# Kernel optimization log

Hardware: AMD Instinct MI355X
Metric: run time of the kernel (lower is better)

The kernel has to match this reference:

```python
import jax, jax.numpy as jnp
import numpy as np

B, L, H = 8, 2048, 1024
MASK_IDENTITY = True


def setup_inputs() -> dict:
    key = jax.random.key(0)
    ks = jax.random.split(key, 7)
    s = 1.0 / np.sqrt(H)
    return {
        "x": jax.random.normal(ks[0], (B, L, H), dtype=jnp.float32),
        "Wq": jax.random.uniform(ks[1], (H, H), jnp.float32, -s, s),
        "bq": jax.random.uniform(ks[2], (H,), jnp.float32, -s, s),
        "Wk": jax.random.uniform(ks[3], (H, H), jnp.float32, -s, s),
        "bk": jax.random.uniform(ks[4], (H,), jnp.float32, -s, s),
        "Wv": jax.random.uniform(ks[5], (H, H), jnp.float32, -s, s),
        "bv": jax.random.uniform(ks[6], (H,), jnp.float32, -s, s),
    }


def reference(x, Wq, bq, Wk, bk, Wv, bv):
    # Linear layers (torch Linear: y = x @ W.T + b)
    q = jnp.einsum("blh,oh->blo", x, Wq) + bq
    k = jnp.einsum("blh,oh->blo", x, Wk) + bk
    v = jnp.einsum("blh,oh->blo", x, Wv) + bv
    hidden = q.shape[-1]
    # NOTE: original scales by hidden_size, not sqrt(hidden_size)
    attn = jnp.einsum("blh,bmh->blm", q / hidden, k)  # [B, L, L]
    if MASK_IDENTITY:
        mask_value = -jnp.finfo(attn.dtype).max
        eye = jnp.eye(attn.shape[-1], dtype=bool)  # [L, L]
        attn = jnp.where(eye[None, :, :], mask_value, attn)
    attn = jax.nn.softmax(attn, axis=-1)
    return jnp.einsum("blm,bmh->blh", attn, v)
```

## Files before the change

kernel.cpp:

```cpp
#include <hip/hip_runtime.h>


typedef unsigned short u16;
typedef __bf16 bfx8 __attribute__((ext_vector_type(8)));
typedef float f32x4 __attribute__((ext_vector_type(4)));

__device__ __forceinline__ u16 f2bf(float f) {
    unsigned int x = __float_as_uint(f);
    unsigned int r = (x + 0x7fffu + ((x >> 16) & 1u)) >> 16;
    return (u16)r;
}
__device__ __forceinline__ float bf2f(u16 u) {
    return __uint_as_float(((unsigned int)u) << 16);
}

__global__ void f32_to_bf16(const float* __restrict__ src, u16* __restrict__ dst, int n8) {
    int i = blockIdx.x * blockDim.x + threadIdx.x;
    if (i < n8) {
        float4 a = ((const float4*)src)[i * 2];
        float4 b = ((const float4*)src)[i * 2 + 1];
        ushort4 lo; lo.x = f2bf(a.x); lo.y = f2bf(a.y); lo.z = f2bf(a.z); lo.w = f2bf(a.w);
        ushort4 hi; hi.x = f2bf(b.x); hi.y = f2bf(b.y); hi.z = f2bf(b.z); hi.w = f2bf(b.w);
        ((ushort4*)dst)[i * 2] = lo;
        ((ushort4*)dst)[i * 2 + 1] = hi;
    }
}

__global__ void transpose_bf16(const u16* __restrict__ src, u16* __restrict__ dst) {
    __shared__ u16 s[64][64 + 8];
    int z = blockIdx.z;
    int tm = blockIdx.x * 64;
    int th = blockIdx.y * 64;
    const u16* sp = src + (long)z * 2048 * 1024;
    u16* dp = dst + (long)z * 1024 * 2048;
    int t = threadIdx.x;
#pragma unroll
    for (int p = 0; p < 4; ++p) {
        int r = p * 16 + (t >> 4);
        int c = (t & 15) * 4;
        ushort4 v = *(const ushort4*)(sp + (long)(tm + r) * 1024 + th + c);
        s[r][c] = v.x; s[r][c + 1] = v.y; s[r][c + 2] = v.z; s[r][c + 3] = v.w;
    }
    __syncthreads();
#pragma unroll
    for (int p = 0; p < 4; ++p) {
        int hr = p * 16 + (t >> 4);
        int c = (t & 15) * 4;
        ushort4 v;
        v.x = s[c][hr]; v.y = s[c + 1][hr]; v.z = s[c + 2][hr]; v.w = s[c + 3][hr];
        *(ushort4*)(dp + (long)(th + hr) * 2048 + tm + c) = v;
    }
}


#define FENCE asm volatile("" ::: "memory")
#define BAR   __builtin_amdgcn_s_barrier()
#define PRIO1 __builtin_amdgcn_s_setprio(1)
#define PRIO0 __builtin_amdgcn_s_setprio(0)
#define VMC(N) asm volatile("s_waitcnt vmcnt(" #N ")" ::: "memory")

#define STAGE_HALF(DST, SRC, LD, tt, h) do{ \
    _Pragma("unroll") \
    for (int rnd = 0; rnd < 2; ++rnd) { \
        int c_ = rnd * 512 + tid; \
        int row_ = (h) * 128 + (c_ >> 3); \
        int slot_ = c_ & 7; \
        const u16* g_ = (SRC) + (long)row_ * (LD) + (tt) * 64 + ((slot_ ^ (row_ & 7)) << 3); \
        char* l_ = (char*)(DST) + (h) * 16384 + rnd * 8192 + wid * 1024; \
        __builtin_amdgcn_global_load_lds((__attribute__((address_space(1))) void*)g_, \
            (__attribute__((address_space(3))) void*)l_, 16, 0, 0); \
    } \
}while(0)

#define RD_A4(dst, SARR, mibase) do{ \
    const char* _b = (const char*)(SARR) + ((wr * 128 + (mibase) * 16 + rA) * 128); \
    dst[0][0] = *(const bfx8*)(_b + 0 * 2048 + ofk0); dst[0][1] = *(const bfx8*)(_b + 0 * 2048 + ofk1); \
    dst[1][0] = *(const bfx8*)(_b + 1 * 2048 + ofk0); dst[1][1] = *(const bfx8*)(_b + 1 * 2048 + ofk1); \
    dst[2][0] = *(const bfx8*)(_b + 2 * 2048 + ofk0); dst[2][1] = *(const bfx8*)(_b + 2 * 2048 + ofk1); \
    dst[3][0] = *(const bfx8*)(_b + 3 * 2048 + ofk0); dst[3][1] = *(const bfx8*)(_b + 3 * 2048 + ofk1); \
}while(0)

#define RD_B2(dst, SARR, nibase) do{ \
    const char* _b = (const char*)(SARR) + ((wc * 64 + (nibase) * 16 + rA) * 128); \
    dst[0][0] = *(const bfx8*)(_b + 0 * 2048 + ofk0); dst[0][1] = *(const bfx8*)(_b + 0 * 2048 + ofk1); \
    dst[1][0] = *(const bfx8*)(_b + 1 * 2048 + ofk0); dst[1][1] = *(const bfx8*)(_b + 1 * 2048 + ofk1); \
}while(0)

#define MMQ(AS, BS, M0, N0) do{ \
    _Pragma("unroll") \
    for (int ks = 0; ks < 2; ++ks) \
    _Pragma("unroll") \
    for (int mi = 0; mi < 4; ++mi) \
    _Pragma("unroll") \
    for (int ni = 0; ni < 2; ++ni) \
        acc[(M0)+mi][(N0)+ni] = __builtin_amdgcn_mfma_f32_16x16x32_bf16(AS[mi][ks], BS[ni][ks], acc[(M0)+mi][(N0)+ni], 0, 0, 0); \
}while(0)

#define TILE(SA_c, SB_c, SA_o, SB_o, tt) do{ \
     \
    RD_B2(b01, SB_c, 0); RD_B2(b23, SB_c, 2); \
    if ((tt) + 1 < NT) STAGE_HALF(SB_o, B, ldb, (tt) + 1, 0); \
    FENCE; BAR; PRIO1; MMQ(aA, b01, 0, 0); PRIO0; FENCE; BAR; \
     \
    RD_A4(aB, SA_c, 4); \
    if ((tt) + 1 < NT) STAGE_HALF(SB_o, B, ldb, (tt) + 1, 1); \
    FENCE; BAR; PRIO1; MMQ(aA, b23, 0, 2); PRIO0; FENCE; BAR; \
     \
    if ((tt) + 2 < NT) STAGE_HALF(SA_c, A, lda, (tt) + 2, 0); \
    VMC(6); \
    FENCE; BAR; PRIO1; MMQ(aB, b23, 4, 2); PRIO0; FENCE; BAR; \
     \
    RD_A4(aA, SA_o, 0); \
    if ((tt) + 2 < NT) STAGE_HALF(SA_c, A, lda, (tt) + 2, 1); \
    VMC(4); \
    FENCE; BAR; PRIO1; MMQ(aB, b01, 4, 0); PRIO0; FENCE; BAR; \
}while(0)

template <int MODE>
__global__ __launch_bounds__(512, 2) void gemm8p(
    const u16* __restrict__ Ab, const u16* __restrict__ Bb,
    int K, int lda, int ldb,
    long strideA, long strideB,
    const float* __restrict__ biasCat,
    u16* __restrict__ outBf, long strideP,
    float* __restrict__ den,
    float* __restrict__ outF)
{
    __shared__ __align__(16) u16 sA0[16384];
    __shared__ __align__(16) u16 sB0[16384];
    __shared__ __align__(16) u16 sA1[16384];
    __shared__ __align__(16) u16 sB1[16384];

    const int tid  = threadIdx.x;
    const int lane = tid & 63;
    const int wid  = tid >> 6;
    const int wr = wid >> 2, wc = wid & 3;
    const int z = blockIdx.z;
    const u16* A = Ab + (long)z * strideA + (long)blockIdx.x * 256 * lda;
    const u16* B = Bb + (long)z * strideB + (long)blockIdx.y * 256 * ldb;
    const int NT = K >> 6;

    const int rA  = lane & 15;
    const int cg  = lane >> 4;
    const int swz = rA & 7;
    const int ofk0 = ((cg)     ^ swz) << 4;
    const int ofk1 = ((cg | 4) ^ swz) << 4;

    f32x4 acc[8][4] = {};
    bfx8 aA[4][2], aB[4][2], b01[2][2], b23[2][2];

    STAGE_HALF(sA0, A, lda, 0, 0); STAGE_HALF(sA0, A, lda, 0, 1);
    STAGE_HALF(sB0, B, ldb, 0, 0); STAGE_HALF(sB0, B, ldb, 0, 1);
    STAGE_HALF(sA1, A, lda, 1, 0); STAGE_HALF(sA1, A, lda, 1, 1);
    VMC(4);
    BAR;
    RD_A4(aA, sA0, 0);
    FENCE;

    for (int t = 0; t < NT; t += 2) {
        TILE(sA0, sB0, sA1, sB1, t);
        TILE(sA1, sB1, sA0, sB0, t + 1);
    }

    const int r0 = blockIdx.x * 256 + wr * 128 + (cg << 2);
    const int c0 = blockIdx.y * 256 + wc * 64 + rA;
#pragma unroll
    for (int mi = 0; mi < 8; ++mi) {
#pragma unroll
        for (int r = 0; r < 4; ++r) {
            const int grow = r0 + mi * 16 + r;
            if constexpr (MODE == 0) {
#pragma unroll
                for (int ni = 0; ni < 4; ++ni) {
                    int gcol = c0 + ni * 16;
                    float v = acc[mi][ni][r] + biasCat[gcol];
                    if (gcol < 1024) v *= (1.0f / 1024.0f);
                    int which = gcol >> 10;
                    long dst = (long)which * (16384L * 1024) + (long)grow * 1024 + (gcol & 1023);
                    outBf[dst] = f2bf(v);
                }
            } else if constexpr (MODE == 1) {
                float s = 0.0f;
#pragma unroll
                for (int ni = 0; ni < 4; ++ni) {
                    int gcol = c0 + ni * 16;
                    float p = (grow == gcol) ? 0.0f : __expf(acc[mi][ni][r]);
                    u16 pb = f2bf(p);
                    outBf[(long)z * strideP + (long)grow * 2048 + gcol] = pb;
                    s += bf2f(pb);
                }
                s += __shfl_xor(s, 1); s += __shfl_xor(s, 2);
                s += __shfl_xor(s, 4); s += __shfl_xor(s, 8);
                if (rA == 0) atomicAdd(&den[z * 2048 + grow], s);
            } else {
                float d = den[z * 2048 + grow];
#pragma unroll
                for (int ni = 0; ni < 4; ++ni)
                    outF[(long)z * (2048L * 1024) + (long)grow * 1024 + (c0 + ni * 16)] = acc[mi][ni][r] / d;
            }
        }
    }
}

extern "C" void kernel_launch(void* const* d_in, const int* in_sizes, int n_in,
                              void* d_out, int out_size, void* d_ws, size_t ws_size,
                              hipStream_t stream) {
    const float* x  = (const float*)d_in[0];
    const float* Wq = (const float*)d_in[1];
    const float* bq = (const float*)d_in[2];
    const float* Wk = (const float*)d_in[3];
    const float* bk = (const float*)d_in[4];
    const float* Wv = (const float*)d_in[5];
    const float* bv = (const float*)d_in[6];
    float* out = (float*)d_out;

    const long XB_OFF   = 0;
    const long WB_OFF   = 33554432;
    const long BIAS_OFF = WB_OFF + 6291456;
    const long DEN_OFF  = BIAS_OFF + 12288;
    const long QKV_OFF  = DEN_OFF + 65536;
    const long PB_OFF   = QKV_OFF + 2L * 33554432;
    const unsigned long long NEED = (unsigned long long)(PB_OFF + 67108864);
    if (ws_size < NEED) return;

    char* ws = (char*)d_ws;
    u16*   xb      = (u16*)(ws + XB_OFF);
    u16*   vT      = (u16*)(ws + XB_OFF);
    u16*   Wb      = (u16*)(ws + WB_OFF);
    float* biasCat = (float*)(ws + BIAS_OFF);
    float* den     = (float*)(ws + DEN_OFF);
    u16*   qkv     = (u16*)(ws + QKV_OFF);
    u16*   qb = qkv;
    u16*   kb = qkv + 16384L * 1024;
    u16*   vb = qkv + 2L * 16384 * 1024;
    u16*   Pb = (u16*)(ws + PB_OFF);

    f32_to_bf16<<<8192, 256, 0, stream>>>(x, xb, 2097152);
    f32_to_bf16<<<512, 256, 0, stream>>>(Wq, Wb, 131072);
    f32_to_bf16<<<512, 256, 0, stream>>>(Wk, Wb + 1048576, 131072);
    f32_to_bf16<<<512, 256, 0, stream>>>(Wv, Wb + 2097152, 131072);
    hipMemcpyAsync(biasCat,        bq, 4096, hipMemcpyDeviceToDevice, stream);
    hipMemcpyAsync(biasCat + 1024, bk, 4096, hipMemcpyDeviceToDevice, stream);
    hipMemcpyAsync(biasCat + 2048, bv, 4096, hipMemcpyDeviceToDevice, stream);
    hipMemsetAsync(den, 0, 65536, stream);

    gemm8p<0><<<dim3(64, 12, 1), 512, 0, stream>>>(
        xb, Wb, 1024, 1024, 1024, 0, 0, biasCat, qkv, 0, nullptr, nullptr);

    transpose_bf16<<<dim3(32, 16, 8), 256, 0, stream>>>(vb, vT);

    gemm8p<1><<<dim3(8, 8, 8), 512, 0, stream>>>(
        qb, kb, 1024, 1024, 1024, 2048L * 1024, 2048L * 1024,
        nullptr, Pb, 2048L * 2048, den, nullptr);

    gemm8p<2><<<dim3(8, 4, 8), 512, 0, stream>>>(
        Pb, vT, 2048, 2048, 2048, 2048L * 2048, 1024L * 2048,
        nullptr, nullptr, 0, den, out);
}
```

Baseline: 413.8 us.

## Compute V transposed directly via swapped GEMM, reorder tile pipeline, remap workgroups

Drops the separate V transpose kernel and instead computes V^T with a new GEMM mode that swaps operands (Wv times x), writing a bf16 transposed output with per-row bias. The main GEMM loop is also reordered: B fragments are prefetched one step earlier and the vmcnt waits are moved. The LDS swizzle gains an extra XOR bit to cut bank conflicts, and workgroup IDs are remapped in groups of eight for better L2/XCD locality. The workspace layout changes so Pb reuses the xb region. This risks correctness in the new swizzle and wait counts, and the QK projection grid shrinks from 12 to 8 column tiles.

After: 519.5 us. 25.6% more time.

```diff
diff --git a/kernel.cpp b/kernel.cpp
--- a/kernel.cpp
+++ b/kernel.cpp
@@ -26,33 +26,6 @@
     }
 }
 
-__global__ void transpose_bf16(const u16* __restrict__ src, u16* __restrict__ dst) {
-    __shared__ u16 s[64][64 + 8];
-    int z = blockIdx.z;
-    int tm = blockIdx.x * 64;
-    int th = blockIdx.y * 64;
-    const u16* sp = src + (long)z * 2048 * 1024;
-    u16* dp = dst + (long)z * 1024 * 2048;
-    int t = threadIdx.x;
-#pragma unroll
-    for (int p = 0; p < 4; ++p) {
-        int r = p * 16 + (t >> 4);
-        int c = (t & 15) * 4;
-        ushort4 v = *(const ushort4*)(sp + (long)(tm + r) * 1024 + th + c);
-        s[r][c] = v.x; s[r][c + 1] = v.y; s[r][c + 2] = v.z; s[r][c + 3] = v.w;
-    }
-    __syncthreads();
-#pragma unroll
-    for (int p = 0; p < 4; ++p) {
-        int hr = p * 16 + (t >> 4);
-        int c = (t & 15) * 4;
-        ushort4 v;
-        v.x = s[c][hr]; v.y = s[c + 1][hr]; v.z = s[c + 2][hr]; v.w = s[c + 3][hr];
-        *(ushort4*)(dp + (long)(th + hr) * 2048 + tm + c) = v;
-    }
-}
-
-
 #define FENCE asm volatile("" ::: "memory")
 #define BAR   __builtin_amdgcn_s_barrier()
 #define PRIO1 __builtin_amdgcn_s_setprio(1)
@@ -64,8 +37,8 @@
     for (int rnd = 0; rnd < 2; ++rnd) { \
         int c_ = rnd * 512 + tid; \
         int row_ = (h) * 128 + (c_ >> 3); \
-        int slot_ = c_ & 7; \
-        const u16* g_ = (SRC) + (long)row_ * (LD) + (tt) * 64 + ((slot_ ^ (row_ & 7)) << 3); \
+        int sg_ = (c_ & 7) ^ (row_ & 7) ^ ((c_ >> 6) & 1); \
+        const u16* g_ = (SRC) + (long)row_ * (LD) + (tt) * 64 + (sg_ << 3); \
         char* l_ = (char*)(DST) + (h) * 16384 + rnd * 8192 + wid * 1024; \
         __builtin_amdgcn_global_load_lds((__attribute__((address_space(1))) void*)g_, \
             (__attribute__((address_space(3))) void*)l_, 16, 0, 0); \
@@ -98,30 +71,29 @@
 
 #define TILE(SA_c, SB_c, SA_o, SB_o, tt) do{ \
      \
-    RD_B2(b01, SB_c, 0); RD_B2(b23, SB_c, 2); \
+    RD_B2(b23, SB_c, 2); \
     if ((tt) + 1 < NT) STAGE_HALF(SB_o, B, ldb, (tt) + 1, 0); \
-    FENCE; BAR; PRIO1; MMQ(aA, b01, 0, 0); PRIO0; FENCE; BAR; \
+    FENCE; BAR; PRIO1; MMQ(aA, b01, 0, 0); PRIO0; VMC(6); FENCE; BAR; \
      \
     RD_A4(aB, SA_c, 4); \
     if ((tt) + 1 < NT) STAGE_HALF(SB_o, B, ldb, (tt) + 1, 1); \
-    FENCE; BAR; PRIO1; MMQ(aA, b23, 0, 2); PRIO0; FENCE; BAR; \
-     \
+    FENCE; BAR; PRIO1; MMQ(aA, b23, 0, 2); PRIO0; VMC(4); FENCE; BAR; \
+     \
+    RD_A4(aA, SA_o, 0); \
     if ((tt) + 2 < NT) STAGE_HALF(SA_c, A, lda, (tt) + 2, 0); \
-    VMC(6); \
-    FENCE; BAR; PRIO1; MMQ(aB, b23, 4, 2); PRIO0; FENCE; BAR; \
-     \
-    RD_A4(aA, SA_o, 0); \
+    FENCE; BAR; PRIO1; MMQ(aB, b01, 4, 0); PRIO0; VMC(2); FENCE; BAR; \
+     \
+    RD_B2(b01, SB_o, 0); \
     if ((tt) + 2 < NT) STAGE_HALF(SA_c, A, lda, (tt) + 2, 1); \
-    VMC(4); \
-    FENCE; BAR; PRIO1; MMQ(aB, b01, 4, 0); PRIO0; FENCE; BAR; \
+    FENCE; BAR; PRIO1; MMQ(aB, b23, 4, 2); PRIO0; VMC(4); FENCE; BAR; \
 }while(0)
 
 template <int MODE>
-__global__ __launch_bounds__(512, 2) void gemm8p(
+__global__ __launch_bounds__(512, 2) void gemm(
     const u16* __restrict__ Ab, const u16* __restrict__ Bb,
     int K, int lda, int ldb,
     long strideA, long strideB,
-    const float* __restrict__ biasCat,
+    const float* __restrict__ bias,
     u16* __restrict__ outBf, long strideP,
     float* __restrict__ den,
     float* __restrict__ outF)
@@ -136,13 +108,20 @@
     const int wid  = tid >> 6;
     const int wr = wid >> 2, wc = wid & 3;
     const int z = blockIdx.z;
-    const u16* A = Ab + (long)z * strideA + (long)blockIdx.x * 256 * lda;
-    const u16* B = Bb + (long)z * strideB + (long)blockIdx.y * 256 * ldb;
+
+    const int nx = gridDim.x;
+    int orig = blockIdx.y * nx + blockIdx.x;
+    int nwg  = nx * gridDim.y;
+    int wg   = (nwg & 7) ? orig : ((orig & 7) * (nwg >> 3) + (orig >> 3));
+    const int bx = wg % nx, by = wg / nx;
+
+    const u16* A = Ab + (long)z * strideA + (long)bx * 256 * lda;
+    const u16* B = Bb + (long)z * strideB + (long)by * 256 * ldb;
     const int NT = K >> 6;
 
     const int rA  = lane & 15;
     const int cg  = lane >> 4;
-    const int swz = rA & 7;
+    const int swz = (rA & 7) ^ (rA >> 3);
     const int ofk0 = ((cg)     ^ swz) << 4;
     const int ofk1 = ((cg | 4) ^ swz) << 4;
 
@@ -155,6 +134,7 @@
     VMC(4);
     BAR;
     RD_A4(aA, sA0, 0);
+    RD_B2(b01, sB0, 0);
     FENCE;
 
     for (int t = 0; t < NT; t += 2) {
@@ -162,8 +142,8 @@
         TILE(sA1, sB1, sA0, sB0, t + 1);
     }
 
-    const int r0 = blockIdx.x * 256 + wr * 128 + (cg << 2);
-    const int c0 = blockIdx.y * 256 + wc * 64 + rA;
+    const int r0 = bx * 256 + wr * 128 + (cg << 2);
+    const int c0 = by * 256 + wc * 64 + rA;
 #pragma unroll
     for (int mi = 0; mi < 8; ++mi) {
 #pragma unroll
@@ -173,7 +153,7 @@
 #pragma unroll
                 for (int ni = 0; ni < 4; ++ni) {
                     int gcol = c0 + ni * 16;
-                    float v = acc[mi][ni][r] + biasCat[gcol];
+                    float v = acc[mi][ni][r] + bias[gcol];
                     if (gcol < 1024) v *= (1.0f / 1024.0f);
                     int which = gcol >> 10;
                     long dst = (long)which * (16384L * 1024) + (long)grow * 1024 + (gcol & 1023);
@@ -192,11 +172,19 @@
                 s += __shfl_xor(s, 1); s += __shfl_xor(s, 2);
                 s += __shfl_xor(s, 4); s += __shfl_xor(s, 8);
                 if (rA == 0) atomicAdd(&den[z * 2048 + grow], s);
-            } else {
+            } else if constexpr (MODE == 2) {
                 float d = den[z * 2048 + grow];
 #pragma unroll
                 for (int ni = 0; ni < 4; ++ni)
                     outF[(long)z * (2048L * 1024) + (long)grow * 1024 + (c0 + ni * 16)] = acc[mi][ni][r] / d;
+            } else {
+                float bv = bias[grow];
+#pragma unroll
+                for (int ni = 0; ni < 4; ++ni) {
+                    int gcol = c0 + ni * 16;
+                    long dst = (long)(gcol >> 11) * (1024L * 2048) + (long)grow * 2048 + (gcol & 2047);
+                    outBf[dst] = f2bf(acc[mi][ni][r] + bv);
+                }
             }
         }
     }
@@ -216,44 +204,45 @@
 
     const long XB_OFF   = 0;
     const long WB_OFF   = 33554432;
-    const long BIAS_OFF = WB_OFF + 6291456;
-    const long DEN_OFF  = BIAS_OFF + 12288;
-    const long QKV_OFF  = DEN_OFF + 65536;
-    const long PB_OFF   = QKV_OFF + 2L * 33554432;
-    const unsigned long long NEED = (unsigned long long)(PB_OFF + 67108864);
+    const long PB_OFF   = 0;
+    const long BIAS_OFF = 67108864;
+    const long DEN_OFF  = BIAS_OFF + 16384;
+    const long QK_OFF   = DEN_OFF + 65536;
+    const long VT_OFF   = QK_OFF + 2L * 33554432;
+    const unsigned long long NEED = (unsigned long long)(VT_OFF + 33554432);
     if (ws_size < NEED) return;
 
     char* ws = (char*)d_ws;
     u16*   xb      = (u16*)(ws + XB_OFF);
-    u16*   vT      = (u16*)(ws + XB_OFF);
     u16*   Wb      = (u16*)(ws + WB_OFF);
-    float* biasCat = (float*)(ws + BIAS_OFF);
+    u16*   Pb      = (u16*)(ws + PB_OFF);
+    float* biasQK  = (float*)(ws + BIAS_OFF);
+    float* biasV   = (float*)(ws + BIAS_OFF + 8192);
     float* den     = (float*)(ws + DEN_OFF);
-    u16*   qkv     = (u16*)(ws + QKV_OFF);
-    u16*   qb = qkv;
-    u16*   kb = qkv + 16384L * 1024;
-    u16*   vb = qkv + 2L * 16384 * 1024;
-    u16*   Pb = (u16*)(ws + PB_OFF);
+    u16*   qb      = (u16*)(ws + QK_OFF);
+    u16*   kb      = qb + 16384L * 1024;
+    u16*   vT      = (u16*)(ws + VT_OFF);
 
     f32_to_bf16<<<8192, 256, 0, stream>>>(x, xb, 2097152);
     f32_to_bf16<<<512, 256, 0, stream>>>(Wq, Wb, 131072);
     f32_to_bf16<<<512, 256, 0, stream>>>(Wk, Wb + 1048576, 131072);
     f32_to_bf16<<<512, 256, 0, stream>>>(Wv, Wb + 2097152, 131072);
-    hipMemcpyAsync(biasCat,        bq, 4096, hipMemcpyDeviceToDevice, stream);
-    hipMemcpyAsync(biasCat + 1024, bk, 4096, hipMemcpyDeviceToDevice, stream);
-    hipMemcpyAsync(biasCat + 2048, bv, 4096, hipMemcpyDeviceToDevice, stream);
+    hipMemcpyAsync(biasQK,        bq, 4096, hipMemcpyDeviceToDevice, stream);
+    hipMemcpyAsync(biasQK + 1024, bk, 4096, hipMemcpyDeviceToDevice, stream);
+    hipMemcpyAsync(biasV,         bv, 4096, hipMemcpyDeviceToDevice, stream);
     hipMemsetAsync(den, 0, 65536, stream);
 
-    gemm8p<0><<<dim3(64, 12, 1), 512, 0, stream>>>(
-        xb, Wb, 1024, 1024, 1024, 0, 0, biasCat, qkv, 0, nullptr, nullptr);
-
-    transpose_bf16<<<dim3(32, 16, 8), 256, 0, stream>>>(vb, vT);
-
-    gemm8p<1><<<dim3(8, 8, 8), 512, 0, stream>>>(
+    gemm<0><<<dim3(64, 8, 1), 512, 0, stream>>>(
+        xb, Wb, 1024, 1024, 1024, 0, 0, biasQK, qb, 0, nullptr, nullptr);
+
+    gemm<3><<<dim3(4, 64, 1), 512, 0, stream>>>(
+        Wb + 2097152, xb, 1024, 1024, 1024, 0, 0, biasV, vT, 0, nullptr, nullptr);
+
+    gemm<1><<<dim3(8, 8, 8), 512, 0, stream>>>(
         qb, kb, 1024, 1024, 1024, 2048L * 1024, 2048L * 1024,
         nullptr, Pb, 2048L * 2048, den, nullptr);
 
-    gemm8p<2><<<dim3(8, 4, 8), 512, 0, stream>>>(
+    gemm<2><<<dim3(8, 4, 8), 512, 0, stream>>>(
         Pb, vT, 2048, 2048, 2048, 2048L * 2048, 1024L * 2048,
         nullptr, nullptr, 0, den, out);
 }
```
